# Kernel optimization log

Hardware: AMD Instinct MI355X
Metric: run time of the kernel (lower is better)

The kernel has to match this reference:

```python
import math
import jax, jax.numpy as jnp
from jax import lax
import numpy as np

NUM_ANG_BINS = 8
NUM_SPATIAL_BINS = 4
SPATIAL_BIN_SIZE = 4
CLIPVAL = 0.2
STRIDE = 1
PAD = 1
EPS = 1e-10
DN = ('NCHW', 'OIHW', 'NCHW')


def _sift_pooling_kernel(ksize: int) -> np.ndarray:
    ks_2 = float(ksize) / 2.0
    xc2 = ks_2 - np.abs(np.arange(ksize, dtype=np.float32) + 0.5 - ks_2)
    return np.outer(xc2, xc2) / ks_2 ** 2  # (ksize, ksize)


def _reshape_kernel(kd: int, ky: int, kx: int) -> np.ndarray:
    numel = kd * ky * kx
    return np.eye(numel, dtype=np.float32).reshape(numel, kd, ky, kx)


def setup_inputs() -> dict:
    key = jax.random.key(0)
    x = jax.random.uniform(key, (2, 1, 512, 512), dtype=jnp.float32)
    pool_kernel = jnp.asarray(_sift_pooling_kernel(SPATIAL_BIN_SIZE))[None, None]  # (1,1,4,4)
    reshape_kernel = jnp.asarray(
        _reshape_kernel(NUM_ANG_BINS, NUM_SPATIAL_BINS, NUM_SPATIAL_BINS))  # (128,8,4,4)
    return {"x": x, "pool_kernel": pool_kernel, "reshape_kernel": reshape_kernel}


def _l2norm_c(t):
    # F.normalize(t, p=2, dim=1)
    n = jnp.sqrt(jnp.sum(t * t, axis=1, keepdims=True))
    return t / jnp.maximum(n, 1e-12)


def reference(x, pool_kernel, reshape_kernel):
    nbins = NUM_ANG_BINS
    two_pi = 2.0 * math.pi
    # spatial_gradient(mode='diff', normalized=True): central diff / 2 with replicate pad
    xp = jnp.pad(x, ((0, 0), (0, 0), (1, 1), (1, 1)), mode='edge')
    gx = 0.5 * (xp[:, :, 1:-1, 2:] - xp[:, :, 1:-1, :-2])
    gy = 0.5 * (xp[:, :, 2:, 1:-1] - xp[:, :, :-2, 1:-1])
    mag = jnp.sqrt(gx * gx + gy * gy + EPS)
    ori = jnp.arctan2(gy, gx + EPS) + two_pi
    o_big = nbins * ori / two_pi
    bo0f = jnp.floor(o_big)
    wo1 = o_big - bo0f
    bo0 = (bo0f.astype(jnp.int32) % nbins)[:, 0]          # (B,H,W)
    bo1 = (bo0 + 1) % nbins
    w0 = ((1.0 - wo1) * mag)[:, 0]                        # (B,H,W)
    w1 = (wo1 * mag)[:, 0]
    # soft-bin the magnitude into angular channels (vectorized over bins)
    ang = (jax.nn.one_hot(bo0, nbins, axis=1, dtype=x.dtype) * w0[:, None] +
           jax.nn.one_hot(bo1, nbins, axis=1, dtype=x.dtype) * w1[:, None])  # (B,8,H,W)
    # depthwise triangular pooling, padding ksize//2 -> (B,8,H+1,W+1)
    p = SPATIAL_BIN_SIZE // 2
    dw = jnp.tile(pool_kernel, (nbins, 1, 1, 1))  # (8,1,4,4)
    pooled = lax.conv_general_dilated(ang, dw, (1, 1), ((p, p), (p, p)),
                                      dimension_numbers=DN, feature_group_count=nbins)
    # neigh2channels identity conv -> (B,128,H,W)
    out = lax.conv_general_dilated(pooled, reshape_kernel, (STRIDE, STRIDE),
                                   ((PAD, PAD), (PAD, PAD)), dimension_numbers=DN)
    out = jnp.clip(_l2norm_c(out), 0.0, CLIPVAL)
    out = _l2norm_c(out)
    # RootSIFT
    n1 = jnp.maximum(jnp.sum(jnp.abs(out), axis=1, keepdims=True), 1e-12)
    out = jnp.sqrt(out / n1 + EPS)
    return out
```

## Files before the change

### kernel.cpp

```cpp
#include <hip/hip_runtime.h>
#include <hip/hip_fp16.h>
#include <math.h>

#define TY 4
#define TX 64
#define AH (TY + 6)
#define AW (TX + 6)
#define PH (TY + 3)
#define PW (TX + 3)
#define H 512
#define W 512
#define HW (H * W)

#define ANGX_OFF 0
#define ANG_OFF  21440
#define POOL_OFF 21440
#define SMEM_BYTES 36448

__device__ __forceinline__ unsigned short f2h(float f) {
    return __half_as_ushort(__float2half(f));
}
__device__ __forceinline__ float h2f_lo(unsigned int u) {
    return __half2float(__ushort_as_half((unsigned short)(u & 0xffffu)));
}
__device__ __forceinline__ float h2f_hi(unsigned int u) {
    return __half2float(__ushort_as_half((unsigned short)(u >> 16)));
}

__global__ __launch_bounds__(256, 4) void sift_kernel(const float* __restrict__ x,
                                                      float* __restrict__ out) {
    __shared__ __align__(16) char smem[SMEM_BYTES];
    float4* s_angx = (float4*)(smem + ANGX_OFF);
    uint4*  s_ang  = (uint4*)(smem + ANG_OFF);
    float4* s_pool = (float4*)(smem + POOL_OFF);

    const int tid = threadIdx.x;
    const int x0 = blockIdx.x * TX;
    const int y0 = blockIdx.y * TY;
    const int b  = blockIdx.z;
    const float* __restrict__ xb = x + (size_t)b * HW;

    const float K1[4] = {0.25f, 0.75f, 0.75f, 0.25f};

    for (int i = tid; i < AH * AW; i += 256) {
        int ay = i / AW, ax = i - ay * AW;
        int gy = y0 - 3 + ay, gx = x0 - 3 + ax;
        float w0 = 0.f, w1 = 0.f;
        int bin = 0;
        if (gy >= 0 && gy < H && gx >= 0 && gx < W) {
            int gxm = gx - 1 < 0 ? 0 : gx - 1;
            int gxp_ = gx + 1 > W - 1 ? W - 1 : gx + 1;
            int gym = gy - 1 < 0 ? 0 : gy - 1;
            int gyp_ = gy + 1 > H - 1 ? H - 1 : gy + 1;
            float gxv = 0.5f * (xb[gy * W + gxp_] - xb[gy * W + gxm]);
            float gyv = 0.5f * (xb[gyp_ * W + gx] - xb[gym * W + gx]);
            float mag = __builtin_amdgcn_sqrtf(gxv * gxv + gyv * gyv + 1e-10f);
            float gxe = gxv + 1e-10f;
            float axv = fabsf(gxe), ayv = fabsf(gyv);
            float mn = fminf(axv, ayv), mx = fmaxf(axv, ayv);
            float t = mn * __builtin_amdgcn_rcpf(fmaxf(mx, 1e-30f));
            float t2 = t * t;
            float p = t * fmaf(t2, fmaf(t2, fmaf(t2, fmaf(t2,
                        fmaf(t2, -0.01492385f, 0.06704027f),
                        -0.14824684f), 0.2464268f), -0.4235113f), 1.2732106f);
            float q = (ayv > axv) ? (2.0f - p) : p;
            q = (gxe < 0.0f) ? (4.0f - q) : q;
            float o = (gyv < 0.0f) ? (0.0f - q) : q;
            float of = floorf(o);
            float wo1 = o - of;
            bin = ((int)of) & 7;
            w0 = (1.f - wo1) * mag;
            w1 = wo1 * mag;
        }
        unsigned short h0 = f2h(w0), h1 = f2h(w1);
        unsigned int pack01 = (unsigned int)h0 | ((unsigned int)h1 << 16);
        unsigned int ph0 = (unsigned int)h0 << 16;
        unsigned int pl1 = (unsigned int)h1;
        int j0 = bin >> 1;
        int j1 = ((bin + 1) & 7) >> 1;
        bool ev = (bin & 1) == 0;
        uint4 d;
        d.x = ev ? (j0 == 0 ? pack01 : 0u) : ((j0 == 0 ? ph0 : 0u) | (j1 == 0 ? pl1 : 0u));
        d.y = ev ? (j0 == 1 ? pack01 : 0u) : ((j0 == 1 ? ph0 : 0u) | (j1 == 1 ? pl1 : 0u));
        d.z = ev ? (j0 == 2 ? pack01 : 0u) : ((j0 == 2 ? ph0 : 0u) | (j1 == 2 ? pl1 : 0u));
        d.w = ev ? (j0 == 3 ? pack01 : 0u) : ((j0 == 3 ? ph0 : 0u) | (j1 == 3 ? pl1 : 0u));
        s_ang[i] = d;
    }
    __syncthreads();

    for (int i = tid; i < AH * PW; i += 256) {
        int ay = i / PW, pxl = i - ay * PW;
        float acc[8] = {0.f, 0.f, 0.f, 0.f, 0.f, 0.f, 0.f, 0.f};
        int base = ay * AW + pxl;
        #pragma unroll
        for (int v = 0; v < 4; ++v) {
            uint4 q = s_ang[base + v];
            float k = K1[v];
            acc[0] = fmaf(k, h2f_lo(q.x), acc[0]);
            acc[1] = fmaf(k, h2f_hi(q.x), acc[1]);
            acc[2] = fmaf(k, h2f_lo(q.y), acc[2]);
            acc[3] = fmaf(k, h2f_hi(q.y), acc[3]);
            acc[4] = fmaf(k, h2f_lo(q.z), acc[4]);
            acc[5] = fmaf(k, h2f_hi(q.z), acc[5]);
            acc[6] = fmaf(k, h2f_lo(q.w), acc[6]);
            acc[7] = fmaf(k, h2f_hi(q.w), acc[7]);
        }
        s_angx[(ay * 2 + 0) * PW + pxl] = make_float4(acc[0], acc[1], acc[2], acc[3]);
        s_angx[(ay * 2 + 1) * PW + pxl] = make_float4(acc[4], acc[5], acc[6], acc[7]);
    }
    __syncthreads();

    for (int i = tid; i < PH * PW * 2; i += 256) {
        int row = i / PW, pxl = i - row * PW;
        int pyl = row >> 1;
        float4 s = make_float4(0.f, 0.f, 0.f, 0.f);
        #pragma unroll
        for (int u = 0; u < 4; ++u) {
            float4 a = s_angx[((pyl + u) * 2 + (row & 1)) * PW + pxl];
            float k = K1[u];
            s.x = fmaf(k, a.x, s.x);
            s.y = fmaf(k, a.y, s.y);
            s.z = fmaf(k, a.z, s.z);
            s.w = fmaf(k, a.w, s.w);
        }
        bool valid = ((unsigned)(y0 - 1 + pyl) <= 512u) && ((unsigned)(x0 - 1 + pxl) <= 512u);
        if (!valid) s = make_float4(0.f, 0.f, 0.f, 0.f);
        s_pool[row * PW + pxl] = s;
    }
    __syncthreads();

    const int w  = tid >> 6;
    const int l  = tid & 63;
    const int dh = l >> 5;
    const int tx = 32 * (w & 1) + (l & 31);
    const int xx = x0 + tx;

    #pragma unroll
    for (int pp = 0; pp < 2; ++pp) {
        const int ty = 2 * pp + (w >> 1);
        const int yy = y0 + ty;
        float4 r[16];
        float ssq = 0.f;
        #pragma unroll
        for (int ky = 0; ky < 4; ++ky) {
            #pragma unroll
            for (int kx = 0; kx < 4; ++kx) {
                float4 t = s_pool[((ty + ky) * 2 + dh) * PW + (tx + kx)];
                r[ky * 4 + kx] = t;
                ssq = fmaf(t.x, t.x, ssq);
                ssq = fmaf(t.y, t.y, ssq);
                ssq = fmaf(t.z, t.z, ssq);
                ssq = fmaf(t.w, t.w, ssq);
            }
        }
        ssq += __shfl_xor(ssq, 32, 64);
        float inv = __builtin_amdgcn_rsqf(fmaxf(ssq, 1e-24f));
        float su = 0.f;
        #pragma unroll
        for (int m = 0; m < 16; ++m) {
            float4 t = r[m];
            t.x = fminf(t.x * inv, 0.2f);
            t.y = fminf(t.y * inv, 0.2f);
            t.z = fminf(t.z * inv, 0.2f);
            t.w = fminf(t.w * inv, 0.2f);
            r[m] = t;
            su += (t.x + t.y) + (t.z + t.w);
        }
        su += __shfl_xor(su, 32, 64);
        float rs = __builtin_amdgcn_rcpf(fmaxf(su, 1e-12f));
        float* __restrict__ op = out + ((size_t)b * 128 + dh * 64) * (size_t)HW
                                     + (size_t)yy * W + xx;
        #pragma unroll
        for (int dd = 0; dd < 4; ++dd) {
            #pragma unroll
            for (int m = 0; m < 16; ++m) {
                float4 t = r[m];
                float comp = (dd == 0) ? t.x : (dd == 1) ? t.y : (dd == 2) ? t.z : t.w;
                float val = __builtin_amdgcn_sqrtf(fmaf(comp, rs, 1e-10f));
                op[(size_t)(dd * 16 + m) * HW] = val;
            }
        }
    }
}

extern "C" void kernel_launch(void* const* d_in, const int* in_sizes, int n_in,
                              void* d_out, int out_size, void* d_ws, size_t ws_size,
                              hipStream_t stream) {
    const float* x = (const float*)d_in[0];
    float* out = (float*)d_out;
    const int B = in_sizes[0] / (H * W);
    dim3 grid(W / TX, H / TY, B);
    dim3 block(256);
    hipLaunchKernelGGL(sift_kernel, grid, block, 0, stream, x, out);
    (void)n_in; (void)out_size; (void)d_ws; (void)ws_size;
}
```

Baseline: 49.51 us.

## Split fused SIFT kernel into pooling pass and epilogue pass via workspace

Splits the single fused kernel in two. The first kernel computes the gradient binning and triangular pooling and writes a 513x513x8 pooled map to the workspace. The second reads that map from global memory and does the normalisation and the 128-channel writes. The intent is to separate the shared-memory-heavy pooling from the store-bound epilogue so the epilogue can run without LDS limits and at higher occupancy. The cost is an extra launch and a round trip through global memory. The fused path stays as a fallback when the workspace is too small.

```diff
diff --git a/kernel.cpp b/kernel.cpp
--- a/kernel.cpp
+++ b/kernel.cpp
@@ -11,6 +11,7 @@
 #define H 512
 #define W 512
 #define HW (H * W)
+#define PDIM 513
 
 #define ANGX_OFF 0
 #define ANG_OFF  21440
@@ -27,21 +28,10 @@
     return __half2float(__ushort_as_half((unsigned short)(u >> 16)));
 }
 
-__global__ __launch_bounds__(256, 4) void sift_kernel(const float* __restrict__ x,
-                                                      float* __restrict__ out) {
-    __shared__ __align__(16) char smem[SMEM_BYTES];
-    float4* s_angx = (float4*)(smem + ANGX_OFF);
-    uint4*  s_ang  = (uint4*)(smem + ANG_OFF);
-    float4* s_pool = (float4*)(smem + POOL_OFF);
-
-    const int tid = threadIdx.x;
-    const int x0 = blockIdx.x * TX;
-    const int y0 = blockIdx.y * TY;
-    const int b  = blockIdx.z;
-    const float* __restrict__ xb = x + (size_t)b * HW;
-
+__device__ __forceinline__ void stages123(const float* __restrict__ xb,
+                                          int x0, int y0, int tid,
+                                          float4* s_angx, uint4* s_ang, float4* s_pool) {
     const float K1[4] = {0.25f, 0.75f, 0.75f, 0.25f};
-
     for (int i = tid; i < AH * AW; i += 256) {
         int ay = i / AW, ax = i - ay * AW;
         int gy = y0 - 3 + ay, gx = x0 - 3 + ax;
@@ -87,7 +77,6 @@
         s_ang[i] = d;
     }
     __syncthreads();
-
     for (int i = tid; i < AH * PW; i += 256) {
         int ay = i / PW, pxl = i - ay * PW;
         float acc[8] = {0.f, 0.f, 0.f, 0.f, 0.f, 0.f, 0.f, 0.f};
@@ -109,7 +98,6 @@
         s_angx[(ay * 2 + 1) * PW + pxl] = make_float4(acc[4], acc[5], acc[6], acc[7]);
     }
     __syncthreads();
-
     for (int i = tid; i < PH * PW * 2; i += 256) {
         int row = i / PW, pxl = i - row * PW;
         int pyl = row >> 1;
@@ -128,6 +116,118 @@
         s_pool[row * PW + pxl] = s;
     }
     __syncthreads();
+}
+
+__global__ __launch_bounds__(256, 4) void sift_pool_kernel(const float* __restrict__ x,
+                                                           float* __restrict__ ws) {
+    __shared__ __align__(16) char smem[SMEM_BYTES];
+    float4* s_angx = (float4*)(smem + ANGX_OFF);
+    uint4*  s_ang  = (uint4*)(smem + ANG_OFF);
+    float4* s_pool = (float4*)(smem + POOL_OFF);
+
+    const int tid = threadIdx.x;
+    const int x0 = blockIdx.x * TX;
+    const int y0 = blockIdx.y * TY;
+    const int b  = blockIdx.z;
+    const float* __restrict__ xb = x + (size_t)b * HW;
+
+    stages123(xb, x0, y0, tid, s_angx, s_ang, s_pool);
+
+    const size_t bbase = (size_t)b * PDIM * PDIM;
+    for (int i = tid; i < 5 * 65 * 2; i += 256) {
+        int dh = i & 1;
+        int j = i >> 1;
+        int pyl = 1 + j / 65;
+        int pxl = 1 + j - (j / 65) * 65;
+        int py = y0 - 1 + pyl;
+        int px = x0 - 1 + pxl;
+        if (py <= 512 && px <= 512) {
+            float4 v = s_pool[(pyl * 2 + dh) * PW + pxl];
+            *(float4*)(ws + (bbase + (size_t)py * PDIM + px) * 8 + dh * 4) = v;
+        }
+    }
+}
+
+__global__ __launch_bounds__(256, 4) void sift_epi_kernel(const float* __restrict__ ws,
+                                                          float* __restrict__ out) {
+    const int tid = threadIdx.x;
+    const int x0 = blockIdx.x * TX;
+    const int y0 = blockIdx.y * TY;
+    const int b  = blockIdx.z;
+    const int w  = tid >> 6;
+    const int l  = tid & 63;
+    const int dh = l >> 5;
+    const int tx = 32 * (w & 1) + (l & 31);
+    const int xx = x0 + tx;
+    const float* __restrict__ pb = ws + (size_t)b * PDIM * PDIM * 8 + dh * 4;
+
+    #pragma unroll
+    for (int pp = 0; pp < 2; ++pp) {
+        const int ty = 2 * pp + (w >> 1);
+        const int yy = y0 + ty;
+        float4 r[16];
+        float ssq = 0.f;
+        #pragma unroll
+        for (int ky = 0; ky < 4; ++ky) {
+            int py = yy - 1 + ky;
+            float my = ((unsigned)py <= 512u) ? 1.f : 0.f;
+            int pyc = py < 0 ? 0 : (py > 512 ? 512 : py);
+            #pragma unroll
+            for (int kx = 0; kx < 4; ++kx) {
+                int px = xx - 1 + kx;
+                float mxm = ((unsigned)px <= 512u) ? 1.f : 0.f;
+                int pxc = px < 0 ? 0 : (px > 512 ? 512 : px);
+                float4 t = *(const float4*)(pb + ((size_t)pyc * PDIM + pxc) * 8);
+                float m = my * mxm;
+                t.x *= m; t.y *= m; t.z *= m; t.w *= m;
+                r[ky * 4 + kx] = t;
+                ssq = fmaf(t.x, t.x, fmaf(t.y, t.y, fmaf(t.z, t.z, fmaf(t.w, t.w, ssq))));
+            }
+        }
+        ssq += __shfl_xor(ssq, 32, 64);
+        float inv = __builtin_amdgcn_rsqf(fmaxf(ssq, 1e-24f));
+        float su = 0.f;
+        #pragma unroll
+        for (int m = 0; m < 16; ++m) {
+            float4 t = r[m];
+            t.x = fminf(t.x * inv, 0.2f);
+            t.y = fminf(t.y * inv, 0.2f);
+            t.z = fminf(t.z * inv, 0.2f);
+            t.w = fminf(t.w * inv, 0.2f);
+            r[m] = t;
+            su += (t.x + t.y) + (t.z + t.w);
+        }
+        su += __shfl_xor(su, 32, 64);
+        float rs = __builtin_amdgcn_rcpf(fmaxf(su, 1e-12f));
+        float* __restrict__ op = out + ((size_t)b * 128 + dh * 64) * (size_t)HW
+                                     + (size_t)yy * W + xx;
+        #pragma unroll
+        for (int dd = 0; dd < 4; ++dd) {
+            #pragma unroll
+            for (int m = 0; m < 16; ++m) {
+                float4 t = r[m];
+                float comp = (dd == 0) ? t.x : (dd == 1) ? t.y : (dd == 2) ? t.z : t.w;
+                float val = __builtin_amdgcn_sqrtf(fmaf(comp, rs, 1e-10f));
+                op[(size_t)(dd * 16 + m) * HW] = val;
+            }
+        }
+    }
+}
+
+__global__ __launch_bounds__(256, 4) void sift_fused_kernel(const float* __restrict__ x,
+                                                            float* __restrict__ out) {
+    __shared__ __align__(16) char smem[SMEM_BYTES];
+    float4* s_angx = (float4*)(smem + ANGX_OFF);
+    uint4*  s_ang  = (uint4*)(smem + ANG_OFF);
+    float4* s_pool = (float4*)(smem + POOL_OFF);
+
+    const int tid = threadIdx.x;
+    const int x0 = blockIdx.x * TX;
+    const int y0 = blockIdx.y * TY;
+    const int b  = blockIdx.z;
+    const float* __restrict__ xb = x + (size_t)b * HW;
+
+    stages123(xb, x0, y0, tid, s_angx, s_ang, s_pool);
 
     const int w  = tid >> 6;
     const int l  = tid & 63;
@@ -191,6 +291,13 @@
     const int B = in_sizes[0] / (H * W);
     dim3 grid(W / TX, H / TY, B);
     dim3 block(256);
-    hipLaunchKernelGGL(sift_kernel, grid, block, 0, stream, x, out);
-    (void)n_in; (void)out_size; (void)d_ws; (void)ws_size;
-}
+    const size_t ws_need = (size_t)B * PDIM * PDIM * 8 * sizeof(float);
+    if (ws_size >= ws_need) {
+        float* ws = (float*)d_ws;
+        hipLaunchKernelGGL(sift_pool_kernel, grid, block, 0, stream, x, ws);
+        hipLaunchKernelGGL(sift_epi_kernel, grid, block, 0, stream, ws, out);
+    } else {
+        hipLaunchKernelGGL(sift_fused_kernel, grid, block, 0, stream, x, out);
+    }
+    (void)n_in; (void)out_size;
+}
```

Result: slower. 81.71 us (+65.1%).
